# Kernel optimization log

Hardware: AMD Instinct MI355X
Metric: run time of the kernel (lower is better)

## Reference

```python
import jax, jax.numpy as jnp
import numpy as np

B, N = 16, 512


def _line_coords(n):
    # Discrete Fourier slice coordinates for all mValues (center=False, ridgelet=False).
    mu = n + n // 2 if n % 2 == 0 else n + 1
    p = 2 if n % 2 == 0 else n
    m = jnp.arange(mu)           # [mu]
    k = jnp.arange(n)            # [N]
    lt = (m < n)[:, None]        # m < N branch mask, [mu, 1]
    # m < N:  row = k,                 col = (k*m) % N
    # m >= N: row = (k*p*(m-N)) % N,   col = k
    row = jnp.where(lt, k[None, :], (k[None, :] * p * (m[:, None] - n)) % n)
    col = jnp.where(lt, (k[None, :] * m[:, None]) % n, k[None, :])
    return row, col  # each [mu, N] int32


def setup_inputs() -> dict:
    key = jax.random.key(0)
    return {"image": jax.random.normal(key, (B, N, N), dtype=jnp.float32)}


def reference(image):
    b, n, _ = image.shape
    row, col = _line_coords(n)                                   # [mu, N]
    dft = jnp.fft.fft2(image.astype(jnp.complex64), norm="ortho")  # [B, N, N] c64
    slices = dft[:, row, col]                                    # gather -> [B, mu, N]
    sino = jnp.fft.ifft(slices, norm="ortho")                    # [B, mu, N] c64
    # complex sinogram returned as stacked (real, imag) float channels
    return jnp.stack([sino.real, sino.imag], axis=-1)            # [B, mu, N, 2]
```

## Files before the change

### kernel.cpp

```cpp
#include <hip/hip_runtime.h>


#define NN 512
#define MU 768
#define MASK 511
#define SCALE 0.04419417382415922f

__global__ __launch_bounds__(256) void k_init(const float* __restrict__ img,
                                              float* __restrict__ A0,
                                              float* __restrict__ B0) {
  const int bx = blockIdx.x, b = blockIdx.y;
  const float* src = img + (size_t)b * NN * NN;
  if (bx < 32) {
    __shared__ float T1[64][65], T2[64][65], T3[64][65];
    const int xt = bx & 7, wt = bx >> 3;
    const int x0 = xt * 64, w0 = wt * 64, x3 = ((xt + 4) & 7) * 64;
    for (int idx = threadIdx.x; idx < 4096; idx += 256) {
      int rr = idx >> 6, cc = idx & 63;
      T1[rr][cc] = src[(x0 + rr) * NN + w0 + cc];
      T2[rr][cc] = src[(x0 + rr) * NN + w0 + 256 + cc];
      T3[rr][cc] = src[(x3 + rr) * NN + w0 + 256 + cc];
    }
    __syncthreads();
    float* dst = A0 + (size_t)b * (512 * NN);
    for (int idx = threadIdx.x; idx < 4096; idx += 256) {
      int wl = idx >> 6, xl = idx & 63;
      float t1 = T1[xl][wl];
      dst[(size_t)(w0 + wl) * NN + x0 + xl]       = t1 + T2[xl][wl];
      dst[(size_t)(256 + w0 + wl) * NN + x0 + xl] = t1 + T3[xl][wl];
    }
  } else {
    const int w0 = (bx - 32) * 32;
    const float4* s4 = (const float4*)src;
    float4* d4 = (float4*)(B0 + (size_t)b * (256 * NN));
    for (int it = 0; it < 16; ++it) {
      int flat = it * 256 + threadIdx.x;
      int row = w0 + (flat >> 7), col = flat & 127;
      float4 u = s4[row * 128 + col], v = s4[(row + 256) * 128 + col];
      u.x += v.x; u.y += v.y; u.z += v.z; u.w += v.w;
      d4[row * 128 + col] = u;
    }
  }
}

__global__ __launch_bounds__(512) void k_pass1(const float* __restrict__ A0,
                                               const float* __restrict__ B0,
                                               float* __restrict__ A1,
                                               float* __restrict__ B1) {
  __shared__ float L[16 * 512];
  const int bx = blockIdx.x, b = blockIdx.y;
  const int t = threadIdx.x;
  const bool isB = bx >= 32;
  const int c = isB ? 0 : (bx >> 4);
  const int w = isB ? (bx - 32) : (bx & 15);
  const float* in = isB ? (B0 + (size_t)b * 256 * NN) : (A0 + (size_t)b * 512 * NN);
  {
    const float4* s4 = (const float4*)in;
    float4* l4 = (float4*)L;
    const int pbase = c * 256 + w;
    for (int it = 0; it < 4; ++it) {
      int flat = it * 512 + t;
      int lrow = flat >> 7, col = flat & 127;
      l4[lrow * 128 + col] = s4[(pbase + 16 * lrow) * 128 + col];
    }
  }
  __syncthreads();
  const int g = t >> 7;
  const int x4 = (t & 127) * 4;
  float* outA = A1 + (size_t)b * 512 * NN;
  float* outB = B1 + (size_t)b * 256 * NN;
  for (int jj = 0; jj < 4; ++jj) {
    const int j = jj * 4 + g;
    const int C = isB ? (2 * j) : (c + 2 * j);
    float4 acc = {0.f, 0.f, 0.f, 0.f};
#pragma unroll
    for (int bb = 0; bb < 16; ++bb) {
      int base = (x4 - C * bb * 16) & MASK;
      float4 v = *(const float4*)&L[bb * 512 + base];
      acc.x += v.x; acc.y += v.y; acc.z += v.z; acc.w += v.w;
    }
    const int orow = isB ? (j * 16 + w) : (C * 16 + w);
    float* op = isB ? outB : outA;
    *(float4*)&op[(size_t)orow * NN + x4] = acc;
  }
}

__global__ __launch_bounds__(512) void k_pass2(const float* __restrict__ A1,
                                               const float* __restrict__ B1,
                                               float2* __restrict__ out) {
  __shared__ float L[16 * 512];
  const int bx = blockIdx.x, b = blockIdx.y;
  const int t = threadIdx.x;
  const bool isB = bx >= 32;
  const int c = isB ? 2 * (bx - 32) : bx;
  const float* in = isB ? (B1 + (size_t)b * 256 * NN + (size_t)(c >> 1) * 16 * NN)
                        : (A1 + (size_t)b * 512 * NN + (size_t)c * 16 * NN);
  {
    const float4* s4 = (const float4*)in;
    float4* l4 = (float4*)L;
    for (int it = 0; it < 4; ++it) l4[it * 512 + t] = s4[it * 512 + t];
  }
  __syncthreads();
  float acc[16];
#pragma unroll
  for (int j = 0; j < 16; ++j) acc[j] = 0.f;
#pragma unroll
  for (int bb = 0; bb < 16; ++bb) {
    int base = (t - c * bb) & MASK;
    const int step = (32 * bb) & MASK;
    const float* row = L + bb * 512;
#pragma unroll
    for (int j = 0; j < 16; ++j) {
      acc[j] += row[base];
      base = (base - step) & MASK;
    }
  }
#pragma unroll
  for (int j = 0; j < 16; ++j) {
    int m = isB ? (512 + (c >> 1) + 16 * j) : (c + 32 * j);
    float2 o; o.x = acc[j] * SCALE; o.y = 0.f;
    out[((size_t)b * MU + m) * NN + t] = o;
  }
}

#define TM 16
#define YT 16
#define LDS_STRIDE 516
__global__ __launch_bounds__(512) void drt_main(const float* __restrict__ img,
                                                float* __restrict__ out) {
  __shared__ float rows[YT * LDS_STRIDE];
  const int b = blockIdx.y;
  const int tile = blockIdx.x;
  const int t = threadIdx.x;
  const bool caseB = (tile >= 32);
  const int a0 = caseB ? (tile - 32) * TM : tile * TM;
  const float* __restrict__ src = img + (size_t)b * (NN * NN);
  const int slope0 = caseB ? (2 * a0) : a0;
  const int dslope = caseB ? 2 : 1;
  float acc[TM];
#pragma unroll
  for (int i = 0; i < TM; ++i) acc[i] = 0.0f;
  for (int y0 = 0; y0 < NN; y0 += YT) {
    __syncthreads();
    if (caseB) {
#pragma unroll
      for (int r = 0; r < YT; ++r) rows[r * LDS_STRIDE + t] = src[(y0 + r) * NN + t];
    } else {
#pragma unroll
      for (int rep = 0; rep < YT; ++rep) {
        int idx = rep * NN + t;
        int xx = idx >> 4, cc = idx & 15;
        rows[cc * LDS_STRIDE + xx] = src[xx * NN + y0 + cc];
      }
    }
    __syncthreads();
#pragma unroll 4
    for (int r = 0; r < YT; ++r) {
      const int v = y0 + r;
      int base = t - slope0 * v;
      const int step = dslope * v;
      const float* __restrict__ rowp = rows + r * LDS_STRIDE;
#pragma unroll
      for (int i = 0; i < TM; ++i) { acc[i] += rowp[base & MASK]; base -= step; }
    }
  }
  const int m = caseB ? (NN + a0) : a0;
  float2* outp = (float2*)out;
#pragma unroll
  for (int i = 0; i < TM; ++i) {
    float2 vv; vv.x = acc[i] * SCALE; vv.y = 0.0f;
    outp[((size_t)b * MU + (m + i)) * NN + t] = vv;
  }
}

extern "C" void kernel_launch(void* const* d_in, const int* in_sizes, int n_in,
                              void* d_out, int out_size, void* d_ws, size_t ws_size,
                              hipStream_t stream) {
  const float* img = (const float*)d_in[0];
  if (ws_size < (size_t)51 * 1024 * 1024) {
    drt_main<<<dim3(48, 16), dim3(512), 0, stream>>>(img, (float*)d_out);
    return;
  }
  float* W  = (float*)d_ws;
  float* A0 = W;
  float* A1 = W + 4194304;
  float* B0 = W + 8388608;
  float* B1 = W + 10485760;

  k_init <<<dim3(40, 16), dim3(256), 0, stream>>>(img, A0, B0);
  k_pass1<<<dim3(48, 16), dim3(512), 0, stream>>>(A0, B0, A1, B1);
  k_pass2<<<dim3(48, 16), dim3(512), 0, stream>>>(A1, B1, (float2*)d_out);
}
```

Measured before the change: 104.4 us.

## Fold B-branch row folding into pass1 and widen init kernel reuse

Removes the B0 intermediate: the caseB fold of rows r and r+256 is now computed directly from the image while loading into shared memory in k_pass1. k_init is restructured so that one 512-thread block handles both x halves of a 64-wide column tile, reusing the loaded tiles for four output blocks, and it uses float4 global loads and stores. Together these cut global traffic and remove one buffer from the workspace, at the cost of extra image reads in pass1 and a smaller init grid of 256 blocks.

```diff
diff --git a/kernel.cpp b/kernel.cpp
--- a/kernel.cpp
+++ b/kernel.cpp
@@ -6,45 +6,52 @@
 #define MASK 511
 #define SCALE 0.04419417382415922f
 
-__global__ __launch_bounds__(256) void k_init(const float* __restrict__ img,
-                                              float* __restrict__ A0,
-                                              float* __restrict__ B0) {
+__global__ __launch_bounds__(512) void k_init(const float* __restrict__ img,
+                                              float* __restrict__ A0) {
+  __shared__ float T[3][64][65];
   const int bx = blockIdx.x, b = blockIdx.y;
+  const int xp = bx >> 2, wt = bx & 3;
+  const int x0 = xp * 64, x1 = x0 + 256, w0 = wt * 64;
   const float* src = img + (size_t)b * NN * NN;
-  if (bx < 32) {
-    __shared__ float T1[64][65], T2[64][65], T3[64][65];
-    const int xt = bx & 7, wt = bx >> 3;
-    const int x0 = xt * 64, w0 = wt * 64, x3 = ((xt + 4) & 7) * 64;
-    for (int idx = threadIdx.x; idx < 4096; idx += 256) {
-      int rr = idx >> 6, cc = idx & 63;
-      T1[rr][cc] = src[(x0 + rr) * NN + w0 + cc];
-      T2[rr][cc] = src[(x0 + rr) * NN + w0 + 256 + cc];
-      T3[rr][cc] = src[(x3 + rr) * NN + w0 + 256 + cc];
-    }
-    __syncthreads();
-    float* dst = A0 + (size_t)b * (512 * NN);
-    for (int idx = threadIdx.x; idx < 4096; idx += 256) {
-      int wl = idx >> 6, xl = idx & 63;
-      float t1 = T1[xl][wl];
-      dst[(size_t)(w0 + wl) * NN + x0 + xl]       = t1 + T2[xl][wl];
-      dst[(size_t)(256 + w0 + wl) * NN + x0 + xl] = t1 + T3[xl][wl];
-    }
-  } else {
-    const int w0 = (bx - 32) * 32;
-    const float4* s4 = (const float4*)src;
-    float4* d4 = (float4*)(B0 + (size_t)b * (256 * NN));
-    for (int it = 0; it < 16; ++it) {
-      int flat = it * 256 + threadIdx.x;
-      int row = w0 + (flat >> 7), col = flat & 127;
-      float4 u = s4[row * 128 + col], v = s4[(row + 256) * 128 + col];
-      u.x += v.x; u.y += v.y; u.z += v.z; u.w += v.w;
-      d4[row * 128 + col] = u;
-    }
-  }
+  float* dst = A0 + (size_t)b * (512 * NN);
+
+  auto load_tile = [&](int tile, int xb, int wb, int idx) {
+    const int r = (idx >> 4) & 63, c4 = (idx & 15) << 2;
+    const float4 v = *(const float4*)&src[(size_t)(xb + r) * NN + wb + c4];
+    T[tile][r][c4]     = v.x;
+    T[tile][r][c4 + 1] = v.y;
+    T[tile][r][c4 + 2] = v.z;
+    T[tile][r][c4 + 3] = v.w;
+  };
+  auto store2 = [&](const float (*Ta)[65], const float (*Tb)[65], int rbase,
+                    int cbase) {
+    for (int idx = threadIdx.x; idx < 1024; idx += 512) {
+      const int wl = idx >> 4, x4 = (idx & 15) << 2;
+      float4 a;
+      a.x = Ta[x4][wl]     + Tb[x4][wl];
+      a.y = Ta[x4 + 1][wl] + Tb[x4 + 1][wl];
+      a.z = Ta[x4 + 2][wl] + Tb[x4 + 2][wl];
+      a.w = Ta[x4 + 3][wl] + Tb[x4 + 3][wl];
+      *(float4*)&dst[(size_t)(rbase + wl) * NN + cbase + x4] = a;
+    }
+  };
+
+  for (int idx = threadIdx.x; idx < 3072; idx += 512) {
+    const int tile = idx >> 10;
+    load_tile(tile, (tile == 2) ? x1 : x0, (tile == 0) ? w0 : w0 + 256, idx);
+  }
+  __syncthreads();
+  store2(T[0], T[1], w0, x0);
+  store2(T[0], T[2], 256 + w0, x0);
+  __syncthreads();
+  for (int idx = threadIdx.x; idx < 1024; idx += 512) load_tile(0, x1, w0, idx);
+  __syncthreads();
+  store2(T[0], T[2], w0, x1);
+  store2(T[0], T[1], 256 + w0, x1);
 }
 
 __global__ __launch_bounds__(512) void k_pass1(const float* __restrict__ A0,
-                                               const float* __restrict__ B0,
+                                               const float* __restrict__ img,
                                                float* __restrict__ A1,
                                                float* __restrict__ B1) {
   __shared__ float L[16 * 512];
@@ -53,9 +60,19 @@
   const bool isB = bx >= 32;
   const int c = isB ? 0 : (bx >> 4);
   const int w = isB ? (bx - 32) : (bx & 15);
-  const float* in = isB ? (B0 + (size_t)b * 256 * NN) : (A0 + (size_t)b * 512 * NN);
-  {
-    const float4* s4 = (const float4*)in;
+  if (isB) {
+    const float4* s4 = (const float4*)(img + (size_t)b * NN * NN);
+    float4* l4 = (float4*)L;
+    for (int it = 0; it < 4; ++it) {
+      int flat = it * 512 + t;
+      int lrow = flat >> 7, col = flat & 127;
+      float4 u = s4[(w + 16 * lrow) * 128 + col];
+      float4 v = s4[(w + 16 * lrow + 256) * 128 + col];
+      u.x += v.x; u.y += v.y; u.z += v.z; u.w += v.w;
+      l4[lrow * 128 + col] = u;
+    }
+  } else {
+    const float4* s4 = (const float4*)(A0 + (size_t)b * 512 * NN);
     float4* l4 = (float4*)L;
     const int pbase = c * 256 + w;
     for (int it = 0; it < 4; ++it) {
@@ -177,17 +194,16 @@
                               void* d_out, int out_size, void* d_ws, size_t ws_size,
                               hipStream_t stream) {
   const float* img = (const float*)d_in[0];
-  if (ws_size < (size_t)51 * 1024 * 1024) {
+  if (ws_size < (size_t)42 * 1024 * 1024) {
     drt_main<<<dim3(48, 16), dim3(512), 0, stream>>>(img, (float*)d_out);
     return;
   }
   float* W  = (float*)d_ws;
   float* A0 = W;
   float* A1 = W + 4194304;
-  float* B0 = W + 8388608;
-  float* B1 = W + 10485760;
-
-  k_init <<<dim3(40, 16), dim3(256), 0, stream>>>(img, A0, B0);
-  k_pass1<<<dim3(48, 16), dim3(512), 0, stream>>>(A0, B0, A1, B1);
+  float* B1 = W + 8388608;
+
+  k_init <<<dim3(16, 16), dim3(512), 0, stream>>>(img, A0);
+  k_pass1<<<dim3(48, 16), dim3(512), 0, stream>>>(A0, img, A1, B1);
   k_pass2<<<dim3(48, 16), dim3(512), 0, stream>>>(A1, B1, (float2*)d_out);
 }
```

After: 99.03 us. 1.05x faster.
